# Performance work log

Measured on AMD Instinct MI355X. Metric: run time of the kernel, lower is better.

The kernel has to match this reference:

```python
import jax, jax.numpy as jnp
import numpy as np

N, DIM, R, C = 1024, 201, 72, 4


def setup_inputs() -> dict:
    key = jax.random.key(0)
    k1, k2 = jax.random.split(key)
    x = jax.random.normal(k1, (N, DIM, R, C), dtype=jnp.float32)
    labels = jax.random.randint(k2, (N, R, C), 0, 201, dtype=jnp.int64)
    return {"x": x, "labels": labels}


def _parse_top_down(labels, G):
    # Faithful vectorization of the triple python loop:
    #   top  = first row index with a valid label (label < G); empty if none
    #   down = 0 if rows 0->1 is a valid->invalid transition,
    #          else R-1 if last row valid,
    #          else first valid->invalid transition index; empty if no valid row.
    # (top empty <=> down empty <=> no valid row; then both forced to 0)
    R = labels.shape[1]
    valid = labels < G                              # [n, R, C]
    any_valid = valid.any(axis=1)                   # [n, C]
    first_valid = jnp.argmax(valid, axis=1)         # [n, C]
    trans = valid[:, :-1] & ~valid[:, 1:]           # [n, R-1, C] valid->invalid
    any_trans = trans.any(axis=1)
    first_trans = jnp.argmax(trans, axis=1)
    down = jnp.where(trans[:, 0], 0,
                     jnp.where(valid[:, -1], R - 1,
                               jnp.where(any_trans, first_trans, 0)))
    top = jnp.where(any_valid, first_valid, 0)
    down = jnp.where(any_valid, down, 0)
    return top, down                                # [n, C] each


def _lane_loss(x, labels):
    n, dim, R, C = x.shape
    G = dim - 1
    # softmax-weighted expected grid position per (image, row, lane)
    p = jax.nn.softmax(x[:, :G], axis=1)
    emb = jnp.arange(G, dtype=x.dtype).reshape(1, G, 1, 1)
    pos = jnp.sum(p * emb, axis=1)                  # [n, R, C]

    top, down = _parse_top_down(labels, G)

    # second difference across lanes: d_i - d_{i+1} = pos_i - 2 pos_{i+1} + pos_{i+2}
    dd = jnp.abs(pos[:, :, :-2] - 2.0 * pos[:, :, 1:-1] + pos[:, :, 2:])  # [n, R, C-2]
    rows = jnp.arange(R)

    def side(lane_lo, lane_hi, col_lo, col_hi):
        t = jnp.max(top[:, lane_lo:lane_hi], axis=1)   # [n]
        d = jnp.min(down[:, lane_lo:lane_hi], axis=1)  # [n]
        active = t < d
        W = (d - t + 1).astype(x.dtype)                # segment length
        mask = ((rows[None, :] >= t[:, None]) & (rows[None, :] <= d[:, None])).astype(x.dtype)
        s = jnp.einsum('nr,nrc->n', mask, dd[:, :, col_lo:col_hi])
        Wsafe = jnp.where(active, W, 1.0)
        npairs = float(col_hi - col_lo)                # == C-3 pairs of diffs
        # L1 mean over W rows, then /W again, then / (num pairs)
        loss = jnp.where(active, s / (Wsafe * Wsafe) / npairs, 0.0)
        w = jnp.where(active, W, 0.0)
        return loss, w, active

    loss_l, w_l, left = side(0, 3, 0, C - 3)
    loss_r, w_r, right = side(1, 4, 1, C - 2)
    denom = jnp.where(left & right, 2.0 * R, float(R))
    loss_k = (loss_l * w_l + loss_r * w_r) / denom     # [n]
    flag = jnp.sum((loss_k != 0).astype(jnp.int32))
    total = jnp.sum(loss_k)
    return jnp.where(flag > 0, total / flag.astype(x.dtype), jnp.asarray(0.0, x.dtype))


def reference(x, labels):
    return _lane_loss(x, labels)
```

## Files before the change

### kernel.cpp

```cpp
#include <hip/hip_runtime.h>

#define NIMG  1024
#define DIMX  201
#define GVAL  200
#define RROW  72
#define CLN   4
#define COLS  (RROW * CLN)
#define NSL   4

__global__ __launch_bounds__(COLS) void lane_loss_main(
    const float* __restrict__ x, const int* __restrict__ labels,
    float* __restrict__ total, int* __restrict__ flag,
    int* __restrict__ done, float* __restrict__ out)
{
    __shared__ float s_lds[NSL][COLS];
    __shared__ float w_lds[NSL][COLS];
    __shared__ float pos_s[COLS];
    __shared__ unsigned char valid_s[COLS];
    __shared__ int td_s[8];

    const int n   = blockIdx.x;
    const int tid = threadIdx.x;

    valid_s[tid] = (labels[n * COLS + tid] < GVAL) ? 1 : 0;
    __syncthreads();

    if (tid < CLN) {
        const int c = tid;
        bool any_valid = false; int first_valid = 0;
        bool any_trans = false; int first_trans = 0;
        bool trans0 = false;
        bool v_prev = (valid_s[c] != 0);
        if (v_prev) { any_valid = true; first_valid = 0; }
        for (int r = 1; r < RROW; ++r) {
            bool v = (valid_s[r * CLN + c] != 0);
            if (v && !any_valid) { any_valid = true; first_valid = r; }
            bool tr = v_prev && !v;
            if (tr && !any_trans) { any_trans = true; first_trans = r - 1; }
            if (r == 1) trans0 = tr;
            v_prev = v;
        }
        bool valid_last = v_prev;
        int down;
        if (trans0)          down = 0;
        else if (valid_last) down = RROW - 1;
        else if (any_trans)  down = first_trans;
        else                 down = 0;
        int top = any_valid ? first_valid : 0;
        if (!any_valid) down = 0;
        td_s[c]     = top;
        td_s[4 + c] = down;
    }
    __syncthreads();

    const int t_l = max(td_s[0], max(td_s[1], td_s[2]));
    const int d_l = min(td_s[4], min(td_s[5], td_s[6]));
    const int t_r = max(td_s[1], max(td_s[2], td_s[3]));
    const int d_r = min(td_s[5], min(td_s[6], td_s[7]));
    const bool aL = (t_l < d_l), aR = (t_r < d_r);

    int rmin = RROW, rmax = -1;
    if (aL) { rmin = t_l; rmax = d_l; }
    if (aR) { rmin = min(rmin, t_r); rmax = max(rmax, d_r); }

    if (rmax >= 0) {
        const int ngroups = rmax - rmin + 1;
        const int nact    = NSL * ngroups;

        if (tid < nact) {
            const int slice = tid / ngroups;
            const int g     = tid - slice * ngroups;
            const float* xp = x + (size_t)n * (DIMX * COLS) + (size_t)(rmin + g) * CLN;
            float4 sa = make_float4(0.f, 0.f, 0.f, 0.f);
            float4 wa = make_float4(0.f, 0.f, 0.f, 0.f);
            float df = (float)slice;
            #pragma unroll 10
            for (int d = slice; d < GVAL; d += NSL) {
                float4 v = *(const float4*)(xp + (size_t)d * COLS);
                float ex = __expf(v.x), ey = __expf(v.y),
                      ez = __expf(v.z), ew = __expf(v.w);
                sa.x += ex;                sa.y += ey;
                sa.z += ez;                sa.w += ew;
                wa.x = fmaf(df, ex, wa.x); wa.y = fmaf(df, ey, wa.y);
                wa.z = fmaf(df, ez, wa.z); wa.w = fmaf(df, ew, wa.w);
                df += (float)NSL;
            }
            ((float4*)s_lds[slice])[g] = sa;
            ((float4*)w_lds[slice])[g] = wa;
        }
        __syncthreads();

        if (tid < nact) {
            float st = s_lds[0][tid] + s_lds[1][tid] + s_lds[2][tid] + s_lds[3][tid];
            float wt = w_lds[0][tid] + w_lds[1][tid] + w_lds[2][tid] + w_lds[3][tid];
            pos_s[tid] = wt / st;
        }
        __syncthreads();

        if (tid < 64) {
            float sl = 0.f, sr = 0.f;
            for (int r = rmin + tid; r <= rmax; r += 64) {
                const int lr_ = r - rmin;
                float p0 = pos_s[lr_ * 4 + 0];
                float p1 = pos_s[lr_ * 4 + 1];
                float p2 = pos_s[lr_ * 4 + 2];
                float p3 = pos_s[lr_ * 4 + 3];
                float ddl = fabsf(p0 - 2.f * p1 + p2);
                float ddr = fabsf(p1 - 2.f * p2 + p3);
                if (r >= t_l && r <= d_l) sl += ddl;
                if (r >= t_r && r <= d_r) sr += ddr;
            }
            #pragma unroll
            for (int off = 32; off > 0; off >>= 1) {
                sl += __shfl_down(sl, off, 64);
                sr += __shfl_down(sr, off, 64);
            }
            if (tid == 0) {
                float WL = (float)(d_l - t_l + 1);
                float WR = (float)(d_r - t_r + 1);
                float ll = aL ? (sl / WL) : 0.f;
                float lr = aR ? (sr / WR) : 0.f;
                float denom = (aL && aR) ? (2.f * (float)RROW) : (float)RROW;
                float lk = (ll + lr) / denom;
                if (lk != 0.f) {
                    atomicAdd(total, lk);
                    atomicAdd(flag, 1);
                }
            }
        }
    }

    if (tid == 0) {
        __threadfence();
        if (atomicAdd(done, 1) == NIMG - 1) {
            float tot = atomicAdd(total, 0.f);
            int   f   = atomicAdd(flag, 0);
            out[0] = (f > 0) ? (tot / (float)f) : 0.f;
        }
    }
}

extern "C" void kernel_launch(void* const* d_in, const int* in_sizes, int n_in,
                              void* d_out, int out_size, void* d_ws, size_t ws_size,
                              hipStream_t stream)
{
    const float* x      = (const float*)d_in[0];
    const int*   labels = (const int*)d_in[1];
    float*       out    = (float*)d_out;

    float* total = (float*)d_ws;
    int*   flag  = (int*)((char*)d_ws + sizeof(float));
    int*   done  = (int*)((char*)d_ws + 2 * sizeof(float));

    hipMemsetAsync(d_ws, 0, 3 * sizeof(float), stream);

    lane_loss_main<<<NIMG, COLS, 0, stream>>>(x, labels, total, flag, done, out);
}
```

Before: 368.3 us.

## Split softmax reduction over dim chunks into separate partial and finalize kernels

The per-image kernel becomes a partial kernel launched with five blocks per image, each covering a 40-wide chunk of the softmax dimension. Each block loads ten float4 values per thread up front and accumulates the exp sums and weighted sums into global arrays with atomics. A second kernel then computes the positions and the loss. This is meant to raise parallelism and memory-level concurrency over the single block per image. The cost is a larger workspace memset, global atomics, label parsing done twice, and an extra kernel launch.

After: 368.5 us. About the same (+0.1%).

```diff
diff --git a/kernel.cpp b/kernel.cpp
--- a/kernel.cpp
+++ b/kernel.cpp
@@ -6,25 +6,16 @@
 #define RROW  72
 #define CLN   4
 #define COLS  (RROW * CLN)
-#define NSL   4
-
-__global__ __launch_bounds__(COLS) void lane_loss_main(
-    const float* __restrict__ x, const int* __restrict__ labels,
-    float* __restrict__ total, int* __restrict__ flag,
-    int* __restrict__ done, float* __restrict__ out)
-{
-    __shared__ float s_lds[NSL][COLS];
-    __shared__ float w_lds[NSL][COLS];
-    __shared__ float pos_s[COLS];
-    __shared__ unsigned char valid_s[COLS];
-    __shared__ int td_s[8];
-
-    const int n   = blockIdx.x;
-    const int tid = threadIdx.x;
-
-    valid_s[tid] = (labels[n * COLS + tid] < GVAL) ? 1 : 0;
-    __syncthreads();
-
+#define NCH   5
+#define DCH   40
+#define DSL   10
+
+#define S_ACC_OFF 16
+#define ACC_BYTES (NIMG * COLS * 4)
+
+__device__ __forceinline__ void parse_lanes(const unsigned char* valid_s,
+                                            int* td_s, int tid)
+{
     if (tid < CLN) {
         const int c = tid;
         bool any_valid = false; int first_valid = 0;
@@ -51,6 +42,24 @@
         td_s[c]     = top;
         td_s[4 + c] = down;
     }
+}
+
+__global__ __launch_bounds__(COLS, 6) void lane_partial(
+    const float* __restrict__ x, const int* __restrict__ labels,
+    float* __restrict__ s_acc, float* __restrict__ w_acc)
+{
+    __shared__ float s_lds[4][COLS];
+    __shared__ float w_lds[4][COLS];
+    __shared__ unsigned char valid_s[COLS];
+    __shared__ int td_s[8];
+
+    const int n   = blockIdx.x / NCH;
+    const int ch  = blockIdx.x - n * NCH;
+    const int tid = threadIdx.x;
+
+    valid_s[tid] = (labels[n * COLS + tid] < GVAL) ? 1 : 0;
+    __syncthreads();
+    parse_lanes(valid_s, td_s, tid);
     __syncthreads();
 
     const int t_l = max(td_s[0], max(td_s[1], td_s[2]));
@@ -62,38 +71,82 @@
     int rmin = RROW, rmax = -1;
     if (aL) { rmin = t_l; rmax = d_l; }
     if (aR) { rmin = min(rmin, t_r); rmax = max(rmax, d_r); }
+    if (rmax < 0) return;
+
+    const int ngroups = rmax - rmin + 1;
+    const int nact    = 4 * ngroups;
+
+    if (tid < nact) {
+        const int slice = tid / ngroups;
+        const int g     = tid - slice * ngroups;
+        const int dbase = ch * DCH + slice * DSL;
+        const float* xp = x + (size_t)n * (DIMX * COLS)
+                            + (size_t)dbase * COLS + (rmin + g) * CLN;
+        float4 v[DSL];
+        #pragma unroll
+        for (int j = 0; j < DSL; ++j)
+            v[j] = *(const float4*)(xp + (size_t)j * COLS);
+
+        float4 sa = make_float4(0.f, 0.f, 0.f, 0.f);
+        float4 wa = make_float4(0.f, 0.f, 0.f, 0.f);
+        float df = (float)dbase;
+        #pragma unroll
+        for (int j = 0; j < DSL; ++j) {
+            float ex = __expf(v[j].x), ey = __expf(v[j].y),
+                  ez = __expf(v[j].z), ew = __expf(v[j].w);
+            sa.x += ex;                sa.y += ey;
+            sa.z += ez;                sa.w += ew;
+            wa.x = fmaf(df, ex, wa.x); wa.y = fmaf(df, ey, wa.y);
+            wa.z = fmaf(df, ez, wa.z); wa.w = fmaf(df, ew, wa.w);
+            df += 1.f;
+        }
+        ((float4*)s_lds[slice])[g] = sa;
+        ((float4*)w_lds[slice])[g] = wa;
+    }
+    __syncthreads();
+
+    if (tid < nact) {
+        float st = s_lds[0][tid] + s_lds[1][tid] + s_lds[2][tid] + s_lds[3][tid];
+        float wt = w_lds[0][tid] + w_lds[1][tid] + w_lds[2][tid] + w_lds[3][tid];
+        const int col = n * COLS + rmin * CLN + tid;
+        atomicAdd(&s_acc[col], st);
+        atomicAdd(&w_acc[col], wt);
+    }
+}
+
+__global__ __launch_bounds__(COLS) void lane_finalize(
+    const int* __restrict__ labels,
+    const float* __restrict__ s_acc, const float* __restrict__ w_acc,
+    float* __restrict__ total, int* __restrict__ flag,
+    int* __restrict__ done, float* __restrict__ out)
+{
+    __shared__ float pos_s[COLS];
+    __shared__ unsigned char valid_s[COLS];
+    __shared__ int td_s[8];
+
+    const int n   = blockIdx.x;
+    const int tid = threadIdx.x;
+
+    valid_s[tid] = (labels[n * COLS + tid] < GVAL) ? 1 : 0;
+    __syncthreads();
+    parse_lanes(valid_s, td_s, tid);
+    __syncthreads();
+
+    const int t_l = max(td_s[0], max(td_s[1], td_s[2]));
+    const int d_l = min(td_s[4], min(td_s[5], td_s[6]));
+    const int t_r = max(td_s[1], max(td_s[2], td_s[3]));
+    const int d_r = min(td_s[5], min(td_s[6], td_s[7]));
+    const bool aL = (t_l < d_l), aR = (t_r < d_r);
+
+    int rmin = RROW, rmax = -1;
+    if (aL) { rmin = t_l; rmax = d_l; }
+    if (aR) { rmin = min(rmin, t_r); rmax = max(rmax, d_r); }
 
     if (rmax >= 0) {
-        const int ngroups = rmax - rmin + 1;
-        const int nact    = NSL * ngroups;
-
+        const int nact = 4 * (rmax - rmin + 1);
         if (tid < nact) {
-            const int slice = tid / ngroups;
-            const int g     = tid - slice * ngroups;
-            const float* xp = x + (size_t)n * (DIMX * COLS) + (size_t)(rmin + g) * CLN;
-            float4 sa = make_float4(0.f, 0.f, 0.f, 0.f);
-            float4 wa = make_float4(0.f, 0.f, 0.f, 0.f);
-            float df = (float)slice;
-            #pragma unroll 10
-            for (int d = slice; d < GVAL; d += NSL) {
-                float4 v = *(const float4*)(xp + (size_t)d * COLS);
-                float ex = __expf(v.x), ey = __expf(v.y),
-                      ez = __expf(v.z), ew = __expf(v.w);
-                sa.x += ex;                sa.y += ey;
-                sa.z += ez;                sa.w += ew;
-                wa.x = fmaf(df, ex, wa.x); wa.y = fmaf(df, ey, wa.y);
-                wa.z = fmaf(df, ez, wa.z); wa.w = fmaf(df, ew, wa.w);
-                df += (float)NSL;
-            }
-            ((float4*)s_lds[slice])[g] = sa;
-            ((float4*)w_lds[slice])[g] = wa;
-        }
-        __syncthreads();
-
-        if (tid < nact) {
-            float st = s_lds[0][tid] + s_lds[1][tid] + s_lds[2][tid] + s_lds[3][tid];
-            float wt = w_lds[0][tid] + w_lds[1][tid] + w_lds[2][tid] + w_lds[3][tid];
-            pos_s[tid] = wt / st;
+            const int col = n * COLS + rmin * CLN + tid;
+            pos_s[tid] = w_acc[col] / s_acc[col];
         }
         __syncthreads();
 
@@ -149,10 +202,14 @@
     float*       out    = (float*)d_out;
 
     float* total = (float*)d_ws;
-    int*   flag  = (int*)((char*)d_ws + sizeof(float));
-    int*   done  = (int*)((char*)d_ws + 2 * sizeof(float));
-
-    hipMemsetAsync(d_ws, 0, 3 * sizeof(float), stream);
-
-    lane_loss_main<<<NIMG, COLS, 0, stream>>>(x, labels, total, flag, done, out);
-}
+    int*   flag  = (int*)((char*)d_ws + 4);
+    int*   done  = (int*)((char*)d_ws + 8);
+    float* s_acc = (float*)((char*)d_ws + S_ACC_OFF);
+    float* w_acc = (float*)((char*)d_ws + S_ACC_OFF + ACC_BYTES);
+
+    hipMemsetAsync(d_ws, 0, S_ACC_OFF + 2 * (size_t)ACC_BYTES, stream);
+
+    lane_partial<<<NIMG * NCH, COLS, 0, stream>>>(x, labels, s_acc, w_acc);
+    lane_finalize<<<NIMG, COLS, 0, stream>>>(labels, s_acc, w_acc,
+                                             total, flag, done, out);
+}
```
